# Kernel tuning notes

Measured on AMD Instinct MI355X. Metric: run time of the kernel, lower is better.

## Reference

```python
import jax, jax.numpy as jnp
import numpy as np

E = 8
DIMS = [512, 1024, 1024, 512]
BATCH = 2048


def _init_w(key, shape):
    a = np.sqrt(6.0 / (shape[-2] * shape[-1]))
    return jax.random.uniform(key, shape, dtype=jnp.float32, minval=-a, maxval=a)


def setup_inputs() -> dict:
    key = jax.random.key(0)
    ks = jax.random.split(key, 8)
    inp = {
        "weight_blend": jax.random.uniform(ks[0], (BATCH, E), dtype=jnp.float32),
        "x": jax.random.normal(ks[1], (BATCH, DIMS[0]), dtype=jnp.float32),
    }
    for i in range(3):
        inp[f"W{i}"] = _init_w(ks[2 + i], (E, DIMS[i + 1], DIMS[i]))
        inp[f"B{i}"] = jnp.zeros((E, DIMS[i + 1], 1), dtype=jnp.float32)
    return inp


def reference(weight_blend, x, W0, B0, W1, B1, W2, B2):
    Ws = [W0, W1, W2]
    Bs = [B0, B1, B2]
    acts = [jax.nn.elu, jax.nn.elu, None]
    for W, B, act in zip(Ws, Bs, acts):
        # dropout p=0 -> identity
        # blended-expert GEMM: sum_e wb[b,e] * (W[e] @ x[b]) == einsum
        t = jnp.einsum("be,eoi,bi->bo", weight_blend, W, x)
        bias = jnp.einsum("be,eo->bo", weight_blend, B[..., 0])
        x = t + bias
        if act is not None:
            x = act(x)
    return x
```

## Files before the change

kernel.cpp:

```cpp
#include <hip/hip_runtime.h>
#include <math.h>

typedef __attribute__((ext_vector_type(8))) short bf16x8;
typedef __attribute__((ext_vector_type(4))) float f32x4;

#define NEXP 8
#define BATCH 2048

__device__ __forceinline__ unsigned short f2bf(float f) {
    union { float f; unsigned u; } v; v.f = f;
    unsigned r = v.u + 0x7FFFu + ((v.u >> 16) & 1u);
    return (unsigned short)(r >> 16);
}

__global__ void cvt_f32_bf16(const float* __restrict__ src,
                             unsigned short* __restrict__ dst, int n4) {
    int i = blockIdx.x * blockDim.x + threadIdx.x;
    if (i >= n4) return;
    float4 v = ((const float4*)src)[i];
    ushort4 o;
    o.x = f2bf(v.x); o.y = f2bf(v.y); o.z = f2bf(v.z); o.w = f2bf(v.w);
    ((ushort4*)dst)[i] = o;
}

__device__ __forceinline__ void gload_lds16(const unsigned short* g, void* lds_dst) {
    __builtin_amdgcn_global_load_lds(
        (const __attribute__((address_space(1))) unsigned int*)g,
        (__attribute__((address_space(3))) unsigned int*)lds_dst,
        16, 0, 0);
}

__global__ __launch_bounds__(256, 2) void moe_mfma(
    const unsigned short* __restrict__ Xb,
    const unsigned short* __restrict__ Wb,
    const float* __restrict__ Bias,
    const float* __restrict__ WBl,
    void* __restrict__ Yout,
    int Din, int Dout, int act, int out_bf16)
{
    __shared__ __align__(16) float lds_f[16384];
    unsigned short* lds_h = (unsigned short*)lds_f;

    const int tid = threadIdx.x;
    const int w   = tid >> 6;
    const int l   = tid & 63;
    const int lh  = l >> 4;
    const int ll  = l & 15;
    const int m0  = blockIdx.y * 64;
    const int n0  = blockIdx.x * 64;
    const int e0  = 2 * w, e1 = 2 * w + 1;

    f32x4 acc0[4][4], acc1[4][4];
    #pragma unroll
    for (int t = 0; t < 4; ++t)
        #pragma unroll
        for (int u = 0; u < 4; ++u)
            #pragma unroll
            for (int i = 0; i < 4; ++i) { acc0[t][u][i] = 0.f; acc1[t][u][i] = 0.f; }

    const int srow = l >> 2;
    const int scol = (l & 3) * 8;

    const unsigned short* xg  = Xb + (size_t)(m0 + w * 16 + srow) * Din + scol;
    const unsigned short* wg0 = Wb + ((size_t)e0 * Dout + n0 + srow) * Din + scol;
    const unsigned short* wg1 = Wb + ((size_t)e1 * Dout + n0 + srow) * Din + scol;
    char* xdst  = (char*)lds_f + w * 1024;
    char* wdst0 = (char*)lds_f + 4096 + e0 * 4096;
    char* wdst1 = (char*)lds_f + 4096 + e1 * 4096;
    const size_t wrowstride = (size_t)16 * Din;

    const int nk = Din >> 5;
    for (int kk = 0; kk < nk; ++kk) {
        const int k0 = kk << 5;
        __syncthreads();
        gload_lds16(xg + k0, xdst);
        #pragma unroll
        for (int j = 0; j < 4; ++j) {
            gload_lds16(wg0 + k0 + (size_t)j * wrowstride, wdst0 + j * 1024);
            gload_lds16(wg1 + k0 + (size_t)j * wrowstride, wdst1 + j * 1024);
        }
        __syncthreads();

        bf16x8 a[4];
        #pragma unroll
        for (int t = 0; t < 4; ++t)
            a[t] = *(const bf16x8*)(lds_h + t * 512 + ll * 32 + lh * 8);
        const unsigned short* wp0 = lds_h + 2048 + e0 * 2048;
        const unsigned short* wp1 = lds_h + 2048 + e1 * 2048;
        #pragma unroll
        for (int u = 0; u < 4; ++u) {
            bf16x8 b0 = *(const bf16x8*)(wp0 + u * 512 + ll * 32 + lh * 8);
            bf16x8 b1 = *(const bf16x8*)(wp1 + u * 512 + ll * 32 + lh * 8);
            #pragma unroll
            for (int t = 0; t < 4; ++t) {
                acc0[t][u] = __builtin_amdgcn_mfma_f32_16x16x32_bf16(a[t], b0, acc0[t][u], 0, 0, 0);
                acc1[t][u] = __builtin_amdgcn_mfma_f32_16x16x32_bf16(a[t], b1, acc1[t][u], 0, 0, 0);
            }
        }
    }
    __syncthreads();

    float b0v[4], b1v[4];
    #pragma unroll
    for (int u = 0; u < 4; ++u) {
        int n = n0 + u * 16 + ll;
        b0v[u] = Bias[(size_t)e0 * Dout + n];
        b1v[u] = Bias[(size_t)e1 * Dout + n];
    }
    float* part = lds_f + w * 4096;
    #pragma unroll
    for (int t = 0; t < 4; ++t) {
        #pragma unroll
        for (int r = 0; r < 4; ++r) {
            const int mloc = t * 16 + lh * 4 + r;
            float2 wbp = ((const float2*)(WBl + (size_t)(m0 + mloc) * NEXP))[w];
            #pragma unroll
            for (int u = 0; u < 4; ++u) {
                float v = wbp.x * (acc0[t][u][r] + b0v[u]) + wbp.y * (acc1[t][u][r] + b1v[u]);
                part[mloc * 64 + u * 16 + ll] = v;
            }
        }
    }
    __syncthreads();

    const int tn    = tid & 15;
    const int nloc  = tn * 4;
    const int mloc0 = (tid >> 4) * 4;
    #pragma unroll
    for (int i = 0; i < 4; ++i) {
        const int mloc = mloc0 + i;
        float4 s = *(const float4*)(lds_f + mloc * 64 + nloc);
        #pragma unroll
        for (int p = 1; p < 4; ++p) {
            float4 q = *(const float4*)(lds_f + p * 4096 + mloc * 64 + nloc);
            s.x += q.x; s.y += q.y; s.z += q.z; s.w += q.w;
        }
        if (act) {
            s.x = s.x > 0.f ? s.x : expm1f(s.x);
            s.y = s.y > 0.f ? s.y : expm1f(s.y);
            s.z = s.z > 0.f ? s.z : expm1f(s.z);
            s.w = s.w > 0.f ? s.w : expm1f(s.w);
        }
        const size_t off = (size_t)(m0 + mloc) * Dout + n0 + nloc;
        if (out_bf16) {
            ushort4 o;
            o.x = f2bf(s.x); o.y = f2bf(s.y); o.z = f2bf(s.z); o.w = f2bf(s.w);
            *(ushort4*)((unsigned short*)Yout + off) = o;
        } else {
            *(float4*)((float*)Yout + off) = s;
        }
    }
}

#define BM 64
#define BN 64
#define BK 16
#define PAD 4

__global__ __launch_bounds__(256) void moe_layer_f32(
    const float* __restrict__ X, const float* __restrict__ W,
    const float* __restrict__ Bias, const float* __restrict__ WB,
    float* __restrict__ Y, int Din, int Dout, int act)
{
    __shared__ float As[BK][BM + PAD];
    __shared__ float Bs[BK][BN + PAD];
    const int tid = threadIdx.x;
    const int tm = tid >> 4, tn = tid & 15;
    const int m0 = blockIdx.y * BM, n0 = blockIdx.x * BN;
    const int lr = tid >> 2, lc = (tid & 3) << 2;
    float acc[4][4] = {};
    const float* xrow  = X  + (size_t)(m0 + lr) * Din;
    const float* wbrow = WB + (size_t)(m0 + lr) * NEXP;
    const float* wrow0 = W  + (size_t)(n0 + lr) * Din;
    for (int e = 0; e < NEXP; ++e) {
        const float wbe = wbrow[e];
        const float* wrow = wrow0 + (size_t)e * Dout * Din;
        for (int k0 = 0; k0 < Din; k0 += BK) {
            float4 av = *(const float4*)(xrow + k0 + lc);
            float4 bv = *(const float4*)(wrow + k0 + lc);
            __syncthreads();
            As[lc+0][lr] = av.x*wbe; As[lc+1][lr] = av.y*wbe;
            As[lc+2][lr] = av.z*wbe; As[lc+3][lr] = av.w*wbe;
            Bs[lc+0][lr] = bv.x; Bs[lc+1][lr] = bv.y;
            Bs[lc+2][lr] = bv.z; Bs[lc+3][lr] = bv.w;
            __syncthreads();
            #pragma unroll
            for (int k = 0; k < BK; ++k) {
                float4 a = *(const float4*)&As[k][tm << 2];
                float4 b = *(const float4*)&Bs[k][tn << 2];
                acc[0][0]+=a.x*b.x; acc[0][1]+=a.x*b.y; acc[0][2]+=a.x*b.z; acc[0][3]+=a.x*b.w;
                acc[1][0]+=a.y*b.x; acc[1][1]+=a.y*b.y; acc[1][2]+=a.y*b.z; acc[1][3]+=a.y*b.w;
                acc[2][0]+=a.z*b.x; acc[2][1]+=a.z*b.y; acc[2][2]+=a.z*b.z; acc[2][3]+=a.z*b.w;
                acc[3][0]+=a.w*b.x; acc[3][1]+=a.w*b.y; acc[3][2]+=a.w*b.z; acc[3][3]+=a.w*b.w;
            }
        }
    }
    #pragma unroll
    for (int im = 0; im < 4; ++im) {
        const int m = m0 + (tm << 2) + im;
        const float* wbm = WB + (size_t)m * NEXP;
        float wv[NEXP];
        #pragma unroll
        for (int e = 0; e < NEXP; ++e) wv[e] = wbm[e];
        #pragma unroll
        for (int in = 0; in < 4; ++in) {
            const int n = n0 + (tn << 2) + in;
            float bsum = 0.f;
            #pragma unroll
            for (int e = 0; e < NEXP; ++e) bsum += wv[e] * Bias[(size_t)e * Dout + n];
            float v = acc[im][in] + bsum;
            if (act) v = v > 0.f ? v : expm1f(v);
            acc[im][in] = v;
        }
        float4 o = make_float4(acc[im][0], acc[im][1], acc[im][2], acc[im][3]);
        *(float4*)(Y + (size_t)m * Dout + n0 + (tn << 2)) = o;
    }
}

extern "C" void kernel_launch(void* const* d_in, const int* in_sizes, int n_in,
                              void* d_out, int out_size, void* d_ws, size_t ws_size,
                              hipStream_t stream)
{
    (void)in_sizes; (void)n_in; (void)out_size;
    const float* wb = (const float*)d_in[0];
    const float* x  = (const float*)d_in[1];
    const float* W0 = (const float*)d_in[2];
    const float* B0 = (const float*)d_in[3];
    const float* W1 = (const float*)d_in[4];
    const float* B1 = (const float*)d_in[5];
    const float* W2 = (const float*)d_in[6];
    const float* B2 = (const float*)d_in[7];
    float* out = (float*)d_out;

    const size_t NW0 = (size_t)8*1024*512, NW1 = (size_t)8*1024*1024, NW2 = (size_t)8*512*1024;
    const size_t NX0 = (size_t)BATCH*512, NX1 = (size_t)BATCH*1024;
    const size_t need = (NW0 + NW1 + NW2 + NX0 + 2 * NX1) * 2;

    if (ws_size >= need) {
        unsigned short* Wb0 = (unsigned short*)d_ws;
        unsigned short* Wb1 = Wb0 + NW0;
        unsigned short* Wb2 = Wb1 + NW1;
        unsigned short* xb0 = Wb2 + NW2;
        unsigned short* xb1 = xb0 + NX0;
        unsigned short* xb2 = xb1 + NX1;
        cvt_f32_bf16<<<NW0/4/256, 256, 0, stream>>>(W0, Wb0, NW0/4);
        cvt_f32_bf16<<<NW1/4/256, 256, 0, stream>>>(W1, Wb1, NW1/4);
        cvt_f32_bf16<<<NW2/4/256, 256, 0, stream>>>(W2, Wb2, NW2/4);
        cvt_f32_bf16<<<NX0/4/256, 256, 0, stream>>>(x,  xb0, NX0/4);
        moe_mfma<<<dim3(1024/64, BATCH/64), 256, 0, stream>>>(xb0, Wb0, B0, wb, xb1, 512,  1024, 1, 1);
        moe_mfma<<<dim3(1024/64, BATCH/64), 256, 0, stream>>>(xb1, Wb1, B1, wb, xb2, 1024, 1024, 1, 1);
        moe_mfma<<<dim3(512/64,  BATCH/64), 256, 0, stream>>>(xb2, Wb2, B2, wb, out, 1024, 512,  0, 0);
    } else {
        float* x1 = (float*)d_ws;
        float* x2 = x1 + (size_t)BATCH * 1024;
        moe_layer_f32<<<dim3(1024/BN, BATCH/BM), 256, 0, stream>>>(x,  W0, B0, wb, x1, 512,  1024, 1);
        moe_layer_f32<<<dim3(1024/BN, BATCH/BM), 256, 0, stream>>>(x1, W1, B1, wb, x2, 1024, 1024, 1);
        moe_layer_f32<<<dim3(512/BN,  BATCH/BM), 256, 0, stream>>>(x2, W2, B2, wb, out, 1024, 512,  0);
    }
}
```

Measured before the change: 231.6 us.

## Fuse conversion kernels and enlarge MFMA tile to 128 rows with 512 threads

Merges the four f32-to-bf16 conversion launches into a single kernel. The MoE GEMM now uses 512-thread blocks covering 128 batch rows, with warps split across M halves and expert pairs. The third layer gets a narrower N tile so it still launches 256 blocks. This doubles reuse of each staged weight tile across rows and reduces launch overhead, at the cost of more LDS per block and a two-phase cross-expert reduction through shared memory.

```diff
diff --git a/kernel.cpp b/kernel.cpp
--- a/kernel.cpp
+++ b/kernel.cpp
@@ -13,11 +13,19 @@
     return (unsigned short)(r >> 16);
 }
 
-__global__ void cvt_f32_bf16(const float* __restrict__ src,
-                             unsigned short* __restrict__ dst, int n4) {
+#define C0 1048576
+#define C1 3145728
+#define C2 4194304
+#define C3 4456448
+__global__ void cvt_all(const float* __restrict__ W0, const float* __restrict__ W1,
+                        const float* __restrict__ W2, const float* __restrict__ x,
+                        unsigned short* __restrict__ dst) {
     int i = blockIdx.x * blockDim.x + threadIdx.x;
-    if (i >= n4) return;
-    float4 v = ((const float4*)src)[i];
+    float4 v;
+    if (i < C0)       v = ((const float4*)W0)[i];
+    else if (i < C1)  v = ((const float4*)W1)[i - C0];
+    else if (i < C2)  v = ((const float4*)W2)[i - C1];
+    else              v = ((const float4*)x)[i - C2];
     ushort4 o;
     o.x = f2bf(v.x); o.y = f2bf(v.y); o.z = f2bf(v.z); o.w = f2bf(v.w);
     ((ushort4*)dst)[i] = o;
@@ -30,7 +38,8 @@
         16, 0, 0);
 }
 
-__global__ __launch_bounds__(256, 2) void moe_mfma(
+template<int NU>
+__global__ __launch_bounds__(512, 2) void moe_mfma2(
     const unsigned short* __restrict__ Xb,
     const unsigned short* __restrict__ Wb,
     const float* __restrict__ Bias,
@@ -38,59 +47,66 @@
     void* __restrict__ Yout,
     int Din, int Dout, int act, int out_bf16)
 {
-    __shared__ __align__(16) float lds_f[16384];
-    unsigned short* lds_h = (unsigned short*)lds_f;
+    constexpr int BN   = 16 * NU;
+    constexpr int STAG = 8192 + NEXP * BN * 64;
+    constexpr int PART = 2 * 128 * BN * 4;
+    constexpr int SMEM = STAG > PART ? STAG : PART;
+    __shared__ __align__(16) char smem[SMEM];
+    float* lds_f = (float*)smem;
 
     const int tid = threadIdx.x;
     const int w   = tid >> 6;
     const int l   = tid & 63;
     const int lh  = l >> 4;
     const int ll  = l & 15;
-    const int m0  = blockIdx.y * 64;
-    const int n0  = blockIdx.x * 64;
-    const int e0  = 2 * w, e1 = 2 * w + 1;
-
-    f32x4 acc0[4][4], acc1[4][4];
+    const int mw  = w & 1;
+    const int ew  = w >> 1;
+    const int e0  = 2 * ew;
+    const int m0  = blockIdx.y * 128;
+    const int n0  = blockIdx.x * BN;
+
+    f32x4 acc0[4][NU], acc1[4][NU];
     #pragma unroll
     for (int t = 0; t < 4; ++t)
         #pragma unroll
-        for (int u = 0; u < 4; ++u)
+        for (int u = 0; u < NU; ++u)
             #pragma unroll
             for (int i = 0; i < 4; ++i) { acc0[t][u][i] = 0.f; acc1[t][u][i] = 0.f; }
 
-    const int srow = l >> 2;
-    const int scol = (l & 3) * 8;
-
-    const unsigned short* xg  = Xb + (size_t)(m0 + w * 16 + srow) * Din + scol;
-    const unsigned short* wg0 = Wb + ((size_t)e0 * Dout + n0 + srow) * Din + scol;
-    const unsigned short* wg1 = Wb + ((size_t)e1 * Dout + n0 + srow) * Din + scol;
-    char* xdst  = (char*)lds_f + w * 1024;
-    char* wdst0 = (char*)lds_f + 4096 + e0 * 4096;
-    char* wdst1 = (char*)lds_f + 4096 + e1 * 4096;
-    const size_t wrowstride = (size_t)16 * Din;
+    constexpr int CPW = 1 + NU;
+    const int prow = l >> 2;
+    const int pcol = (l & 3) * 8;
+    const unsigned short* srcp[CPW];
+    #pragma unroll
+    for (int j = 0; j < CPW; ++j) {
+        const int c = w + 8 * j;
+        if (c < 8) {
+            srcp[j] = Xb + (size_t)(m0 + 16 * c + prow) * Din + pcol;
+        } else {
+            const int e = (c - 8) / NU, r = (c - 8) % NU;
+            srcp[j] = Wb + ((size_t)e * Dout + n0 + 16 * r + prow) * Din + pcol;
+        }
+    }
+
+    const char* wb0p = smem + 8192 + e0 * (BN * 64);
 
     const int nk = Din >> 5;
     for (int kk = 0; kk < nk; ++kk) {
         const int k0 = kk << 5;
         __syncthreads();
-        gload_lds16(xg + k0, xdst);
-        #pragma unroll
-        for (int j = 0; j < 4; ++j) {
-            gload_lds16(wg0 + k0 + (size_t)j * wrowstride, wdst0 + j * 1024);
-            gload_lds16(wg1 + k0 + (size_t)j * wrowstride, wdst1 + j * 1024);
-        }
+        #pragma unroll
+        for (int j = 0; j < CPW; ++j)
+            gload_lds16(srcp[j] + k0, smem + (w + 8 * j) * 1024);
         __syncthreads();
 
         bf16x8 a[4];
         #pragma unroll
         for (int t = 0; t < 4; ++t)
-            a[t] = *(const bf16x8*)(lds_h + t * 512 + ll * 32 + lh * 8);
-        const unsigned short* wp0 = lds_h + 2048 + e0 * 2048;
-        const unsigned short* wp1 = lds_h + 2048 + e1 * 2048;
-        #pragma unroll
-        for (int u = 0; u < 4; ++u) {
-            bf16x8 b0 = *(const bf16x8*)(wp0 + u * 512 + ll * 32 + lh * 8);
-            bf16x8 b1 = *(const bf16x8*)(wp1 + u * 512 + ll * 32 + lh * 8);
+            a[t] = *(const bf16x8*)(smem + (64 * mw + 16 * t + ll) * 64 + lh * 16);
+        #pragma unroll
+        for (int u = 0; u < NU; ++u) {
+            bf16x8 b0 = *(const bf16x8*)(wb0p + (16 * u + ll) * 64 + lh * 16);
+            bf16x8 b1 = *(const bf16x8*)(wb0p + BN * 64 + (16 * u + ll) * 64 + lh * 16);
             #pragma unroll
             for (int t = 0; t < 4; ++t) {
                 acc0[t][u] = __builtin_amdgcn_mfma_f32_16x16x32_bf16(a[t], b0, acc0[t][u], 0, 0, 0);
@@ -100,48 +116,63 @@
     }
     __syncthreads();
 
-    float b0v[4], b1v[4];
-    #pragma unroll
-    for (int u = 0; u < 4; ++u) {
-        int n = n0 + u * 16 + ll;
+    float b0v[NU], b1v[NU];
+    #pragma unroll
+    for (int u = 0; u < NU; ++u) {
+        const int n = n0 + u * 16 + ll;
         b0v[u] = Bias[(size_t)e0 * Dout + n];
-        b1v[u] = Bias[(size_t)e1 * Dout + n];
-    }
-    float* part = lds_f + w * 4096;
-    #pragma unroll
-    for (int t = 0; t < 4; ++t) {
-        #pragma unroll
-        for (int r = 0; r < 4; ++r) {
-            const int mloc = t * 16 + lh * 4 + r;
-            float2 wbp = ((const float2*)(WBl + (size_t)(m0 + mloc) * NEXP))[w];
-            #pragma unroll
-            for (int u = 0; u < 4; ++u) {
-                float v = wbp.x * (acc0[t][u][r] + b0v[u]) + wbp.y * (acc1[t][u][r] + b1v[u]);
-                part[mloc * 64 + u * 16 + ll] = v;
+        b1v[u] = Bias[(size_t)(e0 + 1) * Dout + n];
+    }
+
+    float* buf = lds_f + (ew >> 1) * (128 * BN);
+    if (!(ew & 1)) {
+        #pragma unroll
+        for (int t = 0; t < 4; ++t) {
+            #pragma unroll
+            for (int r = 0; r < 4; ++r) {
+                const int m = 64 * mw + 16 * t + 4 * lh + r;
+                float2 wbp = ((const float2*)(WBl + (size_t)(m0 + m) * NEXP))[ew];
+                #pragma unroll
+                for (int u = 0; u < NU; ++u)
+                    buf[m * BN + u * 16 + ll] =
+                        wbp.x * (acc0[t][u][r] + b0v[u]) + wbp.y * (acc1[t][u][r] + b1v[u]);
             }
         }
     }
     __syncthreads();
-
-    const int tn    = tid & 15;
-    const int nloc  = tn * 4;
-    const int mloc0 = (tid >> 4) * 4;
-    #pragma unroll
-    for (int i = 0; i < 4; ++i) {
-        const int mloc = mloc0 + i;
-        float4 s = *(const float4*)(lds_f + mloc * 64 + nloc);
-        #pragma unroll
-        for (int p = 1; p < 4; ++p) {
-            float4 q = *(const float4*)(lds_f + p * 4096 + mloc * 64 + nloc);
-            s.x += q.x; s.y += q.y; s.z += q.z; s.w += q.w;
-        }
+    if (ew & 1) {
+        #pragma unroll
+        for (int t = 0; t < 4; ++t) {
+            #pragma unroll
+            for (int r = 0; r < 4; ++r) {
+                const int m = 64 * mw + 16 * t + 4 * lh + r;
+                float2 wbp = ((const float2*)(WBl + (size_t)(m0 + m) * NEXP))[ew];
+                #pragma unroll
+                for (int u = 0; u < NU; ++u)
+                    buf[m * BN + u * 16 + ll] +=
+                        wbp.x * (acc0[t][u][r] + b0v[u]) + wbp.y * (acc1[t][u][r] + b1v[u]);
+            }
+        }
+    }
+    __syncthreads();
+
+    constexpr int TPR = 4 * NU;
+    constexpr int RPP = 512 / TPR;
+    const int r0 = tid / TPR;
+    const int c4 = (tid % TPR) * 4;
+    #pragma unroll
+    for (int i = 0; i < 128 / RPP; ++i) {
+        const int m = r0 + RPP * i;
+        float4 s = *(const float4*)(lds_f + m * BN + c4);
+        float4 q = *(const float4*)(lds_f + 128 * BN + m * BN + c4);
+        s.x += q.x; s.y += q.y; s.z += q.z; s.w += q.w;
         if (act) {
             s.x = s.x > 0.f ? s.x : expm1f(s.x);
             s.y = s.y > 0.f ? s.y : expm1f(s.y);
             s.z = s.z > 0.f ? s.z : expm1f(s.z);
             s.w = s.w > 0.f ? s.w : expm1f(s.w);
         }
-        const size_t off = (size_t)(m0 + mloc) * Dout + n0 + nloc;
+        const size_t off = (size_t)(m0 + m) * Dout + n0 + c4;
         if (out_bf16) {
             ushort4 o;
             o.x = f2bf(s.x); o.y = f2bf(s.y); o.z = f2bf(s.z); o.w = f2bf(s.w);
@@ -153,8 +184,8 @@
 }
 
 #define BM 64
-#define BN 64
-#define BK 16
+#define BNF 64
+#define BKF 16
 #define PAD 4
 
 __global__ __launch_bounds__(256) void moe_layer_f32(
@@ -162,11 +193,11 @@
     const float* __restrict__ Bias, const float* __restrict__ WB,
     float* __restrict__ Y, int Din, int Dout, int act)
 {
-    __shared__ float As[BK][BM + PAD];
-    __shared__ float Bs[BK][BN + PAD];
+    __shared__ float As[BKF][BM + PAD];
+    __shared__ float Bs[BKF][BNF + PAD];
     const int tid = threadIdx.x;
     const int tm = tid >> 4, tn = tid & 15;
-    const int m0 = blockIdx.y * BM, n0 = blockIdx.x * BN;
+    const int m0 = blockIdx.y * BM, n0 = blockIdx.x * BNF;
     const int lr = tid >> 2, lc = (tid & 3) << 2;
     float acc[4][4] = {};
     const float* xrow  = X  + (size_t)(m0 + lr) * Din;
@@ -175,7 +206,7 @@
     for (int e = 0; e < NEXP; ++e) {
         const float wbe = wbrow[e];
         const float* wrow = wrow0 + (size_t)e * Dout * Din;
-        for (int k0 = 0; k0 < Din; k0 += BK) {
+        for (int k0 = 0; k0 < Din; k0 += BKF) {
             float4 av = *(const float4*)(xrow + k0 + lc);
             float4 bv = *(const float4*)(wrow + k0 + lc);
             __syncthreads();
@@ -185,7 +216,7 @@
             Bs[lc+2][lr] = bv.z; Bs[lc+3][lr] = bv.w;
             __syncthreads();
             #pragma unroll
-            for (int k = 0; k < BK; ++k) {
+            for (int k = 0; k < BKF; ++k) {
                 float4 a = *(const float4*)&As[k][tm << 2];
                 float4 b = *(const float4*)&Bs[k][tn << 2];
                 acc[0][0]+=a.x*b.x; acc[0][1]+=a.x*b.y; acc[0][2]+=a.x*b.z; acc[0][3]+=a.x*b.w;
@@ -243,18 +274,15 @@
         unsigned short* xb0 = Wb2 + NW2;
         unsigned short* xb1 = xb0 + NX0;
         unsigned short* xb2 = xb1 + NX1;
-        cvt_f32_bf16<<<NW0/4/256, 256, 0, stream>>>(W0, Wb0, NW0/4);
-        cvt_f32_bf16<<<NW1/4/256, 256, 0, stream>>>(W1, Wb1, NW1/4);
-        cvt_f32_bf16<<<NW2/4/256, 256, 0, stream>>>(W2, Wb2, NW2/4);
-        cvt_f32_bf16<<<NX0/4/256, 256, 0, stream>>>(x,  xb0, NX0/4);
-        moe_mfma<<<dim3(1024/64, BATCH/64), 256, 0, stream>>>(xb0, Wb0, B0, wb, xb1, 512,  1024, 1, 1);
-        moe_mfma<<<dim3(1024/64, BATCH/64), 256, 0, stream>>>(xb1, Wb1, B1, wb, xb2, 1024, 1024, 1, 1);
-        moe_mfma<<<dim3(512/64,  BATCH/64), 256, 0, stream>>>(xb2, Wb2, B2, wb, out, 1024, 512,  0, 0);
+        cvt_all<<<C3 / 256, 256, 0, stream>>>(W0, W1, W2, x, Wb0);
+        moe_mfma2<4><<<dim3(16, 16), 512, 0, stream>>>(xb0, Wb0, B0, wb, xb1, 512,  1024, 1, 1);
+        moe_mfma2<4><<<dim3(16, 16), 512, 0, stream>>>(xb1, Wb1, B1, wb, xb2, 1024, 1024, 1, 1);
+        moe_mfma2<2><<<dim3(16, 16), 512, 0, stream>>>(xb2, Wb2, B2, wb, out, 1024, 512,  0, 0);
     } else {
         float* x1 = (float*)d_ws;
         float* x2 = x1 + (size_t)BATCH * 1024;
-        moe_layer_f32<<<dim3(1024/BN, BATCH/BM), 256, 0, stream>>>(x,  W0, B0, wb, x1, 512,  1024, 1);
-        moe_layer_f32<<<dim3(1024/BN, BATCH/BM), 256, 0, stream>>>(x1, W1, B1, wb, x2, 1024, 1024, 1);
-        moe_layer_f32<<<dim3(512/BN,  BATCH/BM), 256, 0, stream>>>(x2, W2, B2, wb, out, 1024, 512,  0);
-    }
-}
+        moe_layer_f32<<<dim3(1024/BNF, BATCH/BM), 256, 0, stream>>>(x,  W0, B0, wb, x1, 512,  1024, 1);
+        moe_layer_f32<<<dim3(1024/BNF, BATCH/BM), 256, 0, stream>>>(x1, W1, B1, wb, x2, 1024, 1024, 1);
+        moe_layer_f32<<<dim3(512/BNF,  BATCH/BM), 256, 0, stream>>>(x2, W2, B2, wb, out, 1024, 512,  0);
+    }
+}
```

After: 236.8 us. 1.02x slower.
